# Kernel optimization log

Hardware: AMD Instinct MI355X
Metric: run time of the kernel (lower is better)

The kernel has to match this reference:

```python
import jax, jax.numpy as jnp
import numpy as np

B, T = 1, 2048
N_HEAD = 16
N_KV_HEAD = 16
N_EMBD = 1024
HEAD_DIM = N_EMBD // N_HEAD  # 64
HD8 = HEAD_DIM // 8          # 8 octonion blocks per head
EPS_RMS = 1e-6


def qconj(q):
    return q * jnp.array([1.0, -1.0, -1.0, -1.0], dtype=q.dtype)


def qmul(q1, q2):
    # Hamilton product, (...,4) x (...,4) -> (...,4)
    w1, x1, y1, z1 = (q1[..., 0], q1[..., 1], q1[..., 2], q1[..., 3])
    w2, x2, y2, z2 = (q2[..., 0], q2[..., 1], q2[..., 2], q2[..., 3])
    return jnp.stack([
        w1 * w2 - x1 * x2 - y1 * y2 - z1 * z2,
        w1 * x2 + x1 * w2 + y1 * z2 - z1 * y2,
        w1 * y2 - x1 * z2 + y1 * w2 + z1 * x2,
        w1 * z2 + x1 * y2 - y1 * x2 + z1 * w2,
    ], axis=-1)


def omul(o1, o2):
    # Cayley-Dickson octonion product, (...,8)
    a, b = o1[..., :4], o1[..., 4:]
    c, d = o2[..., :4], o2[..., 4:]
    first = qmul(a, c) - qmul(qconj(d), b)
    second = qmul(d, a) + qmul(b, qconj(c))
    return jnp.concatenate([first, second], axis=-1)


def oconj(o):
    return jnp.concatenate([qconj(o[..., :4]), -o[..., 4:]], axis=-1)


# Octonion multiplication structure constants: omul(x, y)[k] = x[a] y[p] C[a,p,k]
_EYE8 = jnp.eye(8, dtype=jnp.float32)
C_OCT = jax.vmap(lambda ei: jax.vmap(lambda ej: omul(ei, ej))(_EYE8))(_EYE8)  # (8,8,8)
# Trilinear tensor for omul(omul(q, kc), v):  T3[a,p,q,k] = sum_e C[a,p,e] C[e,q,k]
T3 = jnp.einsum('ape,eqk->apqk', C_OCT, C_OCT)  # (8,8,8,8)


def apply_rotary_emb(x, cos, sin):
    # x: (B, T, H, hd); cos/sin: (1, T, 1, hd//2)
    d = x.shape[-1] // 2
    x1, x2 = x[..., :d], x[..., d:]
    y1 = x1 * cos + x2 * sin
    y2 = x2 * cos - x1 * sin
    return jnp.concatenate([y1, y2], axis=-1)


def rms_norm(x):
    return x * jax.lax.rsqrt(jnp.mean(x * x, axis=-1, keepdims=True) + EPS_RMS)


def setup_inputs() -> dict:
    key = jax.random.key(0)
    ks = jax.random.split(key, 7)
    x = jax.random.normal(ks[0], (B, T, N_EMBD), dtype=jnp.float32)
    cos = jax.random.uniform(ks[1], (1, T, 1, HEAD_DIM // 2), dtype=jnp.float32)
    sin = jax.random.uniform(ks[2], (1, T, 1, HEAD_DIM // 2), dtype=jnp.float32)
    s = 0.02
    Wq = jax.random.normal(ks[3], (N_HEAD * HEAD_DIM, N_EMBD), dtype=jnp.float32) * s
    Wk = jax.random.normal(ks[4], (N_KV_HEAD * HEAD_DIM, N_EMBD), dtype=jnp.float32) * s
    Wv = jax.random.normal(ks[5], (N_KV_HEAD * HEAD_DIM, N_EMBD), dtype=jnp.float32) * s
    Wo = jax.random.normal(ks[6], (N_EMBD, N_EMBD), dtype=jnp.float32) * s
    return {"x": x, "cos": cos, "sin": sin, "Wq": Wq, "Wk": Wk, "Wv": Wv, "Wo": Wo}


def reference(x, cos, sin, Wq, Wk, Wv, Wo):
    Bx, Tx, Cx = x.shape
    q = (x @ Wq.T).reshape(Bx, Tx, N_HEAD, HEAD_DIM)
    k = (x @ Wk.T).reshape(Bx, Tx, N_KV_HEAD, HEAD_DIM)
    v = (x @ Wv.T).reshape(Bx, Tx, N_KV_HEAD, HEAD_DIM)
    q = rms_norm(apply_rotary_emb(q, cos, sin))
    k = rms_norm(apply_rotary_emb(k, cos, sin))
    q = q.transpose(0, 2, 1, 3)  # (B,H,T,hd)
    k = k.transpose(0, 2, 1, 3)
    v = v.transpose(0, 2, 1, 3)

    q_o = q.reshape(Bx, N_HEAD, Tx, HD8, 8)
    k_o = k.reshape(Bx, N_KV_HEAD, Tx, HD8, 8)
    v_o = v.reshape(Bx, N_KV_HEAD, Tx, HD8, 8)
    # F.normalize(p=2, dim=-1): divide by max(||.||, 1e-12)
    k_o = k_o / jnp.maximum(jnp.linalg.norm(k_o, axis=-1, keepdims=True), 1e-12)

    # Scores use the (pre-octonion-normalized) rotary+rms k
    scores = jnp.einsum('bhid,bhjd->bhij', q, k) * (HEAD_DIM ** -0.5)
    mask = jnp.tril(jnp.ones((Tx, Tx), dtype=bool))
    scores = jnp.where(mask, scores, -jnp.inf)
    probs = jax.nn.softmax(scores, axis=-1)  # (B,H,Tq,Tk)

    # y_i = sum_j p_ij * omul(omul(q_i, oconj(k_j)), v_j)
    # omul is bilinear, so pull the j-sum inside:
    # y_i[k] = q_i[a] * T3[a,p,c,k] * (sum_j p_ij kc_j[p] v_j[c])
    kc = oconj(k_o)                                              # (B,H,Tk,M,8)
    KV = jnp.einsum('bhjmp,bhjmq->bhjmpq', kc, v_o)              # (B,H,Tk,M,8,8)
    Z = jnp.einsum('bhij,bhjmpq->bhimpq', probs, KV)             # (B,H,Tq,M,8,8)
    y_o = jnp.einsum('bhima,apqk,bhimpq->bhimk', q_o, T3, Z)     # (B,H,Tq,M,8)

    y = y_o.reshape(Bx, N_HEAD, Tx, HEAD_DIM).transpose(0, 2, 1, 3).reshape(Bx, Tx, Cx)
    return y @ Wo.T
```

## Files before the change

kernel.cpp:

```cpp
#include <hip/hip_runtime.h>

typedef unsigned short u16;
typedef unsigned int u32;

#define T_SEQ 2048
#define NHEAD 16
#define HDIM 64
#define CDIM 1024
#define W_HSTR (512*2048)
#define Z_HSTR (2048*512)

#define SGBITS 0xB2D8741EACC66A00ULL

#define EXP2C 0.18033688011112042f

typedef _Float16 f16x8 __attribute__((ext_vector_type(8)));
typedef float f32x4 __attribute__((ext_vector_type(4)));

__device__ __forceinline__ float h2f(u16 u) { _Float16 h; __builtin_memcpy(&h, &u, 2); return (float)h; }
__device__ __forceinline__ u16 f2h(float f) { _Float16 h = (_Float16)f; u16 u; __builtin_memcpy(&u, &h, 2); return u; }
__device__ __forceinline__ u32 pk(float a, float b) { return (u32)f2h(a) | ((u32)f2h(b) << 16); }

__device__ __forceinline__ void gload16(const u16* g, u16* l) {
    __builtin_amdgcn_global_load_lds((const __attribute__((address_space(1))) u32*)g,
                                     (__attribute__((address_space(3))) u32*)l, 16, 0, 0);
}

template<bool F16OUT>
__device__ __forceinline__ void hgemm_tile(const u16* __restrict__ At, int lda,
                                           const u16* __restrict__ Bt, int ldb, int K,
                                           float* __restrict__ Cf, u16* __restrict__ Ch,
                                           int ldc, float scale, u16* As, u16* Bs) {
    int t = threadIdx.x;
    int wave = t >> 6, l = t & 63;
    int wm = wave & 1, wn = wave >> 1;
    int quad = l >> 4, lr = l & 15;
    f32x4 acc[4][4];
#pragma unroll
    for (int i = 0; i < 4; ++i)
#pragma unroll
        for (int j = 0; j < 4; ++j) acc[i][j] = (f32x4){0.f, 0.f, 0.f, 0.f};
    int acol = quad * 8;
    for (int k0 = 0; k0 < K; k0 += 64) {
#pragma unroll
        for (int j = 0; j < 4; ++j) {
            int d = wave * 4 + j;
            int kb = d >> 3, seg = d & 7;
            size_t roff = (size_t)(seg * 16 + lr);
            int coff = k0 + kb * 32 + acol;
            gload16(At + roff * lda + coff, As + d * 512);
            gload16(Bt + roff * ldb + coff, Bs + d * 512);
        }
        __syncthreads();
#pragma unroll
        for (int kb = 0; kb < 2; ++kb) {
            f16x8 af[4], bf[4];
#pragma unroll
            for (int mi = 0; mi < 4; ++mi) af[mi] = *(const f16x8*)&As[(kb * 8 + wm * 4 + mi) * 512 + l * 8];
#pragma unroll
            for (int ni = 0; ni < 4; ++ni) bf[ni] = *(const f16x8*)&Bs[(kb * 8 + wn * 4 + ni) * 512 + l * 8];
#pragma unroll
            for (int mi = 0; mi < 4; ++mi)
#pragma unroll
                for (int ni = 0; ni < 4; ++ni)
                    acc[mi][ni] = __builtin_amdgcn_mfma_f32_16x16x32_f16(af[mi], bf[ni], acc[mi][ni], 0, 0, 0);
        }
        __syncthreads();
    }
#pragma unroll
    for (int mi = 0; mi < 4; ++mi)
#pragma unroll
        for (int ni = 0; ni < 4; ++ni)
#pragma unroll
            for (int rr = 0; rr < 4; ++rr) {
                int gr = wm * 64 + mi * 16 + quad * 4 + rr;
                int gc = wn * 64 + ni * 16 + lr;
                float v = acc[mi][ni][rr] * scale;
                if (F16OUT) Ch[(size_t)gr * ldc + gc] = f2h(v);
                else Cf[(size_t)gr * ldc + gc] = v;
            }
}

__global__ __launch_bounds__(256) void hgemm_f32(const u16* __restrict__ A, int lda,
                                                 const u16* __restrict__ B, int ldb,
                                                 float* __restrict__ C, int ldc, int K) {
    __shared__ u16 As[8192], Bs[8192];
    int bm = blockIdx.y * 128, bn = blockIdx.x * 128;
    hgemm_tile<false>(A + (size_t)bm * lda, lda, B + (size_t)bn * ldb, ldb, K,
                      C + (size_t)bm * ldc + bn, nullptr, ldc, 1.f, As, Bs);
}

__global__ __launch_bounds__(256) void hgemm_f16(const u16* __restrict__ A, int lda,
                                                 const u16* __restrict__ B, int ldb,
                                                 u16* __restrict__ C, int ldc, int K) {
    __shared__ u16 As[8192], Bs[8192];
    int bm = blockIdx.y * 128, bn = blockIdx.x * 128;
    hgemm_tile<true>(A + (size_t)bm * lda, lda, B + (size_t)bn * ldb, ldb, K,
                     nullptr, C + (size_t)bm * ldc + bn, ldc, 1.f, As, Bs);
}

__global__ __launch_bounds__(256, 2) void flash_pw(const u16* __restrict__ q16,
                                                   const u16* __restrict__ k16,
                                                   const u16* __restrict__ W,
                                                   u16* __restrict__ Z,
                                                   float* __restrict__ lbuf) {
    __shared__ u16 Pl[2][128 * 136];
    int idx = blockIdx.x;
    int rb = 15 - (idx >> 6);
    int i6 = idx & 63;
    int h = ((i6 & 7) << 1) | ((i6 >> 3) & 1);
    int nq = i6 >> 4;
    int t = threadIdx.x;
    int wave = t >> 6, l = t & 63;
    int wm = wave & 1, wn = wave >> 1;
    int quad = l >> 4, lr = l & 15;

    const u16* qbase = q16 + (size_t)(rb * 128 + wm * 64 + lr) * CDIM + h * HDIM + quad * 8;
    f16x8 qa[4][2];
#pragma unroll
    for (int mi = 0; mi < 4; ++mi)
#pragma unroll
        for (int kb = 0; kb < 2; ++kb)
            qa[mi][kb] = *(const f16x8*)(qbase + (size_t)(mi * 16) * CDIM + kb * 32);

    f32x4 accz[4][4];
    f32x4 accl[4];
#pragma unroll
    for (int mi = 0; mi < 4; ++mi) {
        accl[mi] = (f32x4){0.f, 0.f, 0.f, 0.f};
#pragma unroll
        for (int ni = 0; ni < 4; ++ni) accz[mi][ni] = (f32x4){0.f, 0.f, 0.f, 0.f};
    }
    f16x8 ones;
#pragma unroll
    for (int j = 0; j < 8; ++j) ones[j] = (_Float16)1.0f;

    const u16* kbase = k16 + (size_t)(wn * 64 + lr) * CDIM + h * HDIM + quad * 8;
    const u16* Wbase = W + (size_t)h * W_HSTR + (size_t)(nq * 128 + wn * 64 + lr) * T_SEQ + quad * 8;

    auto qk = [&](int cb, f32x4 (&s)[4][4]) {
        f16x8 kf[4][2];
#pragma unroll
        for (int ni = 0; ni < 4; ++ni)
#pragma unroll
            for (int kb = 0; kb < 2; ++kb)
                kf[ni][kb] = *(const f16x8*)(kbase + (size_t)(cb * 128 + ni * 16) * CDIM + kb * 32);
#pragma unroll
        for (int mi = 0; mi < 4; ++mi)
#pragma unroll
            for (int ni = 0; ni < 4; ++ni) s[mi][ni] = (f32x4){0.f, 0.f, 0.f, 0.f};
#pragma unroll
        for (int kb = 0; kb < 2; ++kb)
#pragma unroll
            for (int mi = 0; mi < 4; ++mi)
#pragma unroll
                for (int ni = 0; ni < 4; ++ni)
                    s[mi][ni] = __builtin_amdgcn_mfma_f32_16x16x32_f16(qa[mi][kb], kf[ni][kb], s[mi][ni], 0, 0, 0);
    };
    auto expst = [&](int cb, f32x4 (&s)[4][4], u16* Pd) {
#pragma unroll
        for (int mi = 0; mi < 4; ++mi) {
            int row = wm * 64 + mi * 16 + quad * 4;
#pragma unroll
            for (int ni = 0; ni < 4; ++ni) {
                int col = wn * 64 + ni * 16 + lr;
#pragma unroll
                for (int rr = 0; rr < 4; ++rr) {
                    bool valid = (cb < rb) | (col <= row + rr);
                    float p = valid ? __builtin_amdgcn_exp2f(s[mi][ni][rr] * EXP2C - 12.f) : 0.f;
                    Pd[(row + rr) * 136 + col] = f2h(p);
                }
            }
        }
    };
    auto pw = [&](int cb, const u16* Ps) {
#pragma unroll
        for (int kb = 0; kb < 4; ++kb) {
            f16x8 pf[4], wf[4];
#pragma unroll
            for (int ni = 0; ni < 4; ++ni)
                wf[ni] = *(const f16x8*)(Wbase + (size_t)(ni * 16) * T_SEQ + cb * 128 + kb * 32);
#pragma unroll
            for (int mi = 0; mi < 4; ++mi)
                pf[mi] = *(const f16x8*)&Ps[(wm * 64 + mi * 16 + lr) * 136 + kb * 32 + quad * 8];
#pragma unroll
            for (int mi = 0; mi < 4; ++mi) {
#pragma unroll
                for (int ni = 0; ni < 4; ++ni)
                    accz[mi][ni] = __builtin_amdgcn_mfma_f32_16x16x32_f16(pf[mi], wf[ni], accz[mi][ni], 0, 0, 0);
                if (nq == 0)
                    accl[mi] = __builtin_amdgcn_mfma_f32_16x16x32_f16(pf[mi], ones, accl[mi], 0, 0, 0);
            }
        }
    };

    {
        f32x4 s[4][4];
        qk(0, s);
        expst(0, s, Pl[0]);
    }
    int cur = 0;
    for (int cb = 1; cb <= rb; ++cb) {
        __syncthreads();
        f32x4 s[4][4];
        qk(cb, s);
        pw(cb - 1, Pl[cur]);
        expst(cb, s, Pl[cur ^ 1]);
        cur ^= 1;
    }
    __syncthreads();
    pw(rb, Pl[cur]);

    u16* Zb = Z + (size_t)h * Z_HSTR;
#pragma unroll
    for (int mi = 0; mi < 4; ++mi)
#pragma unroll
        for (int rr = 0; rr < 4; ++rr) {
            int row = rb * 128 + wm * 64 + mi * 16 + quad * 4 + rr;
#pragma unroll
            for (int ni = 0; ni < 4; ++ni) {
                int col = nq * 128 + wn * 64 + ni * 16 + lr;
                Zb[(size_t)row * 512 + col] = f2h(accz[mi][ni][rr]);
            }
        }
    if (nq == 0 && lr == 0) {
#pragma unroll
        for (int mi = 0; mi < 4; ++mi) {
            int row = rb * 128 + wm * 64 + mi * 16 + quad * 4;
            *(f32x4*)(lbuf + h * T_SEQ + row) = accl[mi];
        }
    }
}

__global__ __launch_bounds__(256) void cvt5(const float* __restrict__ x, const float* __restrict__ wq,
                                            const float* __restrict__ wk, const float* __restrict__ wv,
                                            const float* __restrict__ wo,
                                            u16* __restrict__ x16, u16* __restrict__ w16) {
    int z = blockIdx.y;
    size_t base = ((size_t)blockIdx.x * 256 + threadIdx.x) * 8;
    const float* src;
    u16* dst;
    size_t cnt;
    if (z == 0) { src = x; dst = x16; cnt = 2097152; }
    else if (z == 1) { src = wq; dst = w16; cnt = 1048576; }
    else if (z == 2) { src = wk; dst = w16 + 1048576; cnt = 1048576; }
    else if (z == 3) { src = wv; dst = w16 + 2097152; cnt = 1048576; }
    else { src = wo; dst = w16 + 3145728; cnt = 1048576; }
    if (base >= cnt) return;
    float4 f0 = *(const float4*)(src + base);
    float4 f1 = *(const float4*)(src + base + 4);
    uint4 o;
    o.x = pk(f0.x, f0.y); o.y = pk(f0.z, f0.w); o.z = pk(f1.x, f1.y); o.w = pk(f1.z, f1.w);
    *(uint4*)(dst + base) = o;
}

__global__ __launch_bounds__(256) void prep_rope(const u16* __restrict__ qkv,
                                                 u16* __restrict__ q16, u16* __restrict__ k16,
                                                 float* __restrict__ kc,
                                                 const float* __restrict__ cosb, const float* __restrict__ sinb) {
    int wave = threadIdx.x >> 6, lane = threadIdx.x & 63;
    int idx = blockIdx.x * 4 + wave;
    int t = idx >> 4, h = idx & 15;
    int d = lane & 31;
    float cs = cosb[t * 32 + d];
    float sn = sinb[t * 32 + d];
    size_t b3 = (size_t)t * 3072 + h * HDIM;
    size_t b1 = (size_t)t * CDIM + h * HDIM;

    float xq = h2f(qkv[b3 + lane]);
    float oq = __shfl(xq, lane ^ 32);
    float rq = (lane < 32) ? fmaf(xq, cs, oq * sn) : fmaf(xq, cs, -oq * sn);
    float ssq = rq * rq;
#pragma unroll
    for (int m = 1; m < 64; m <<= 1) ssq += __shfl_xor(ssq, m);
    rq *= rsqrtf(ssq * (1.f / 64.f) + 1e-6f);
    q16[b1 + lane] = f2h(rq);

    float xk = h2f(qkv[b3 + 1024 + lane]);
    float ok = __shfl(xk, lane ^ 32);
    float rk = (lane < 32) ? fmaf(xk, cs, ok * sn) : fmaf(xk, cs, -ok * sn);
    float ssk = rk * rk;
#pragma unroll
    for (int m = 1; m < 64; m <<= 1) ssk += __shfl_xor(ssk, m);
    rk *= rsqrtf(ssk * (1.f / 64.f) + 1e-6f);
    k16[b1 + lane] = f2h(rk);

    float s8 = rk * rk;
    s8 += __shfl_xor(s8, 1); s8 += __shfl_xor(s8, 2); s8 += __shfl_xor(s8, 4);
    float sc2 = 1.f / fmaxf(sqrtf(s8), 1e-12f);
    float kcv = rk * sc2;
    if (lane & 7) kcv = -kcv;
    kc[b1 + lane] = kcv;
}

__global__ __launch_bounds__(256) void w_pre(const float* __restrict__ kc, const u16* __restrict__ qkv,
                                             u16* __restrict__ W) {
    __shared__ float kcs[64][65];
    __shared__ float vs[64][65];
    int h = blockIdx.y;
    int j0 = blockIdx.x * 64;
    int t = threadIdx.x;
    int r = t >> 2, cq = (t & 3) * 16;
    const float* kp = kc + (size_t)(j0 + r) * CDIM + h * HDIM + cq;
    const u16* vp = qkv + (size_t)(j0 + r) * 3072 + 2048 + h * HDIM + cq;
#pragma unroll
    for (int u4 = 0; u4 < 4; ++u4) {
        float4 a = *(const float4*)(kp + u4 * 4);
        ushort4 b = *(const ushort4*)(vp + u4 * 4);
        kcs[r][cq + u4 * 4 + 0] = a.x; kcs[r][cq + u4 * 4 + 1] = a.y;
        kcs[r][cq + u4 * 4 + 2] = a.z; kcs[r][cq + u4 * 4 + 3] = a.w;
        vs[r][cq + u4 * 4 + 0] = h2f(b.x); vs[r][cq + u4 * 4 + 1] = h2f(b.y);
        vs[r][cq + u4 * 4 + 2] = h2f(b.z); vs[r][cq + u4 * 4 + 3] = h2f(b.w);
    }
    __syncthreads();
    int j = t & 63, g = t >> 6;
    u16* Wp = W + (size_t)h * W_HSTR + j0 + j;
    for (int ae = g * 16; ae < g * 16 + 16; ++ae) {
        int a = ae >> 3, e = ae & 7;
        u32 mask = 0;
#pragma unroll
        for (int qq = 0; qq < 8; ++qq) {
            int p = a ^ e ^ qq;
            u32 bit = (u32)(((SGBITS >> (a * 8 + p)) ^ (SGBITS >> ((e ^ qq) * 8 + qq))) & 1ULL);
            mask |= bit << qq;
        }
#pragma unroll
        for (int m = 0; m < 8; ++m) {
            float w = 0.f;
#pragma unroll
            for (int qq = 0; qq < 8; ++qq) {
                float t1 = kcs[j][m * 8 + (a ^ e ^ qq)] * vs[j][m * 8 + qq];
                w = ((mask >> qq) & 1) ? (w - t1) : (w + t1);
            }
            Wp[(size_t)(m * 64 + ae) * T_SEQ] = f2h(w);
        }
    }
}

__global__ __launch_bounds__(256) void contract_y(const u16* __restrict__ q16, const u16* __restrict__ Z,
                                                  const float* __restrict__ lbuf, u16* __restrict__ y16) {
    __shared__ u16 zb[4][512];
    int wave = threadIdx.x >> 6, lane = threadIdx.x & 63;
    int idx = blockIdx.x * 4 + wave;
    int i = idx >> 4, h = idx & 15;
    uint4 zv = *(const uint4*)(Z + (size_t)h * Z_HSTR + (size_t)i * 512 + lane * 8);
    *(uint4*)&zb[wave][lane * 8] = zv;
    int m = lane >> 3, e = lane & 7;
    const u16* qp = q16 + (size_t)i * CDIM + h * HDIM + m * 8;
    uint4 qb = *(const uint4*)qp;
    float qv[8];
    qv[0] = h2f(qb.x & 0xffff); qv[1] = h2f(qb.x >> 16);
    qv[2] = h2f(qb.y & 0xffff); qv[3] = h2f(qb.y >> 16);
    qv[4] = h2f(qb.z & 0xffff); qv[5] = h2f(qb.z >> 16);
    qv[6] = h2f(qb.w & 0xffff); qv[7] = h2f(qb.w >> 16);
    float linv = 1.f / lbuf[h * T_SEQ + i];
    __syncthreads();
    float acc = 0.f;
#pragma unroll
    for (int a = 0; a < 8; ++a) acc = fmaf(qv[a], h2f(zb[wave][m * 64 + a * 8 + e]), acc);
    y16[(size_t)i * CDIM + h * HDIM + lane] = f2h(acc * linv);
}

extern "C" void kernel_launch(void* const* d_in, const int* in_sizes, int n_in,
                              void* d_out, int out_size, void* d_ws, size_t ws_size,
                              hipStream_t stream) {
    const float* x = (const float*)d_in[0];
    const float* cosb = (const float*)d_in[1];
    const float* sinb = (const float*)d_in[2];
    const float* Wq = (const float*)d_in[3];
    const float* Wk = (const float*)d_in[4];
    const float* Wv = (const float*)d_in[5];
    const float* Wo = (const float*)d_in[6];
    float* out = (float*)d_out;
    char* base = (char*)d_ws;
    u16* qkv16 = (u16*)base;
    float* kc = (float*)(base + 12582912);
    u16* x16 = (u16*)(base + 20971520);
    u16* w16 = (u16*)(base + 25165824);
    u16* q16 = (u16*)(base + 33554432);
    u16* k16 = (u16*)(base + 37748736);
    u16* y16 = (u16*)(base + 41943040);
    u16* W = (u16*)(base + 46137344);
    u16* Z = (u16*)(base + 79691776);
    float* lbuf = (float*)(base + 113246208);

    cvt5<<<dim3(1024, 5), 256, 0, stream>>>(x, Wq, Wk, Wv, Wo, x16, w16);
    hgemm_f16<<<dim3(24, 16), 256, 0, stream>>>(x16, CDIM, w16, CDIM, qkv16, 3072, CDIM);
    prep_rope<<<T_SEQ * NHEAD / 4, 256, 0, stream>>>(qkv16, q16, k16, kc, cosb, sinb);
    w_pre<<<dim3(32, 16), 256, 0, stream>>>(kc, qkv16, W);
    flash_pw<<<1024, 256, 0, stream>>>(q16, k16, W, Z, lbuf);
    contract_y<<<NHEAD * T_SEQ / 4, 256, 0, stream>>>(q16, Z, lbuf, y16);
    hgemm_f32<<<dim3(8, 16), 256, 0, stream>>>(y16, CDIM, w16 + 3145728, CDIM, out, CDIM, CDIM);
}
```

Before: 304.0 us.

## Halve flash_pw query tile to 64 rows with transposed, XOR-swizzled P staging

Each flash_pw block now covers 64 query rows instead of 128, which doubles the grid to 2048 blocks and halves the per-block register accumulators. QK^T is computed transposed (K as the A operand), so each lane writes 4 contiguous P values as one ushort4 into an XOR-swizzled LDS layout, replacing the padded scalar stores. The aim is more parallelism, less register pressure, better causal load balance and fewer LDS bank conflicts. In exchange, the QK^T work and K/W global loads are duplicated across twice as many blocks.

After: 381.1 us. 1.25x slower.

```diff
diff --git a/kernel.cpp b/kernel.cpp
--- a/kernel.cpp
+++ b/kernel.cpp
@@ -104,29 +104,32 @@
                                                    const u16* __restrict__ W,
                                                    u16* __restrict__ Z,
                                                    float* __restrict__ lbuf) {
-    __shared__ u16 Pl[2][128 * 136];
+    __shared__ u16 Pt[2][64 * 128];
     int idx = blockIdx.x;
-    int rb = 15 - (idx >> 6);
-    int i6 = idx & 63;
-    int h = ((i6 & 7) << 1) | ((i6 >> 3) & 1);
-    int nq = i6 >> 4;
+    int rb = 15 - (idx >> 7);
+    int sub = idx & 127;
+    int h = ((sub & 7) << 1) | ((sub >> 3) & 1);
+    int nq = (sub >> 4) & 3;
+    int ih = sub >> 6;
     int t = threadIdx.x;
     int wave = t >> 6, l = t & 63;
-    int wm = wave & 1, wn = wave >> 1;
     int quad = l >> 4, lr = l & 15;
-
-    const u16* qbase = q16 + (size_t)(rb * 128 + wm * 64 + lr) * CDIM + h * HDIM + quad * 8;
-    f16x8 qa[4][2];
-#pragma unroll
-    for (int mi = 0; mi < 4; ++mi)
+    int wj = wave & 1, wiq = wave >> 1;
+    int wi = wave & 1, wn = wave >> 1;
+    int i0 = rb * 128 + ih * 64;
+
+    const u16* qb = q16 + (size_t)(i0 + wiq * 32 + lr) * CDIM + h * HDIM + quad * 8;
+    f16x8 qa[2][2];
+#pragma unroll
+    for (int ni = 0; ni < 2; ++ni)
 #pragma unroll
         for (int kb = 0; kb < 2; ++kb)
-            qa[mi][kb] = *(const f16x8*)(qbase + (size_t)(mi * 16) * CDIM + kb * 32);
-
-    f32x4 accz[4][4];
-    f32x4 accl[4];
-#pragma unroll
-    for (int mi = 0; mi < 4; ++mi) {
+            qa[ni][kb] = *(const f16x8*)(qb + (size_t)(ni * 16) * CDIM + kb * 32);
+
+    f32x4 accz[2][4];
+    f32x4 accl[2];
+#pragma unroll
+    for (int mi = 0; mi < 2; ++mi) {
         accl[mi] = (f32x4){0.f, 0.f, 0.f, 0.f};
 #pragma unroll
         for (int ni = 0; ni < 4; ++ni) accz[mi][ni] = (f32x4){0.f, 0.f, 0.f, 0.f};
@@ -135,98 +138,105 @@
 #pragma unroll
     for (int j = 0; j < 8; ++j) ones[j] = (_Float16)1.0f;
 
-    const u16* kbase = k16 + (size_t)(wn * 64 + lr) * CDIM + h * HDIM + quad * 8;
+    const u16* kbase = k16 + (size_t)(wj * 64 + lr) * CDIM + h * HDIM + quad * 8;
     const u16* Wbase = W + (size_t)h * W_HSTR + (size_t)(nq * 128 + wn * 64 + lr) * T_SEQ + quad * 8;
 
-    auto qk = [&](int cb, f32x4 (&s)[4][4]) {
+    auto qk = [&](int cb, f32x4 (&s)[4][2]) {
         f16x8 kf[4][2];
 #pragma unroll
-        for (int ni = 0; ni < 4; ++ni)
+        for (int mi = 0; mi < 4; ++mi)
 #pragma unroll
             for (int kb = 0; kb < 2; ++kb)
-                kf[ni][kb] = *(const f16x8*)(kbase + (size_t)(cb * 128 + ni * 16) * CDIM + kb * 32);
+                kf[mi][kb] = *(const f16x8*)(kbase + (size_t)(cb * 128 + mi * 16) * CDIM + kb * 32);
 #pragma unroll
         for (int mi = 0; mi < 4; ++mi)
 #pragma unroll
-            for (int ni = 0; ni < 4; ++ni) s[mi][ni] = (f32x4){0.f, 0.f, 0.f, 0.f};
+            for (int ni = 0; ni < 2; ++ni) s[mi][ni] = (f32x4){0.f, 0.f, 0.f, 0.f};
 #pragma unroll
         for (int kb = 0; kb < 2; ++kb)
 #pragma unroll
             for (int mi = 0; mi < 4; ++mi)
 #pragma unroll
-                for (int ni = 0; ni < 4; ++ni)
-                    s[mi][ni] = __builtin_amdgcn_mfma_f32_16x16x32_f16(qa[mi][kb], kf[ni][kb], s[mi][ni], 0, 0, 0);
+                for (int ni = 0; ni < 2; ++ni)
+                    s[mi][ni] = __builtin_amdgcn_mfma_f32_16x16x32_f16(kf[mi][kb], qa[ni][kb], s[mi][ni], 0, 0, 0);
     };
-    auto expst = [&](int cb, f32x4 (&s)[4][4], u16* Pd) {
+    auto expst = [&](int cb, f32x4 (&s)[4][2], u16* Pd) {
 #pragma unroll
         for (int mi = 0; mi < 4; ++mi) {
-            int row = wm * 64 + mi * 16 + quad * 4;
-#pragma unroll
-            for (int ni = 0; ni < 4; ++ni) {
-                int col = wn * 64 + ni * 16 + lr;
+            int j0 = wj * 64 + mi * 16 + quad * 4;
+            int chunk = j0 >> 3, joff = j0 & 7;
+#pragma unroll
+            for (int ni = 0; ni < 2; ++ni) {
+                int iloc = wiq * 32 + ni * 16 + lr;
+                ushort4 o;
+                u16* pr = (u16*)&o;
 #pragma unroll
                 for (int rr = 0; rr < 4; ++rr) {
-                    bool valid = (cb < rb) | (col <= row + rr);
+                    bool valid = (cb < rb) | ((j0 + rr) <= (ih * 64 + iloc));
                     float p = valid ? __builtin_amdgcn_exp2f(s[mi][ni][rr] * EXP2C - 12.f) : 0.f;
-                    Pd[(row + rr) * 136 + col] = f2h(p);
+                    pr[rr] = f2h(p);
                 }
+                *(ushort4*)&Pd[iloc * 128 + ((chunk ^ (iloc & 15)) << 3) + joff] = o;
             }
         }
     };
     auto pw = [&](int cb, const u16* Ps) {
 #pragma unroll
         for (int kb = 0; kb < 4; ++kb) {
-            f16x8 pf[4], wf[4];
+            f16x8 pf[2], wf[4];
 #pragma unroll
             for (int ni = 0; ni < 4; ++ni)
                 wf[ni] = *(const f16x8*)(Wbase + (size_t)(ni * 16) * T_SEQ + cb * 128 + kb * 32);
 #pragma unroll
-            for (int mi = 0; mi < 4; ++mi)
-                pf[mi] = *(const f16x8*)&Ps[(wm * 64 + mi * 16 + lr) * 136 + kb * 32 + quad * 8];
-#pragma unroll
-            for (int mi = 0; mi < 4; ++mi) {
+            for (int mi = 0; mi < 2; ++mi) {
+                int iloc = wi * 32 + mi * 16 + lr;
+                int chunk = kb * 4 + quad;
+                pf[mi] = *(const f16x8*)&Ps[iloc * 128 + ((chunk ^ (iloc & 15)) << 3)];
+            }
+#pragma unroll
+            for (int mi = 0; mi < 2; ++mi) {
 #pragma unroll
                 for (int ni = 0; ni < 4; ++ni)
                     accz[mi][ni] = __builtin_amdgcn_mfma_f32_16x16x32_f16(pf[mi], wf[ni], accz[mi][ni], 0, 0, 0);
-                if (nq == 0)
+                if (nq == 0 && wn == 0)
                     accl[mi] = __builtin_amdgcn_mfma_f32_16x16x32_f16(pf[mi], ones, accl[mi], 0, 0, 0);
             }
         }
     };
 
     {
-        f32x4 s[4][4];
+        f32x4 s[4][2];
         qk(0, s);
-        expst(0, s, Pl[0]);
+        expst(0, s, Pt[0]);
     }
     int cur = 0;
     for (int cb = 1; cb <= rb; ++cb) {
         __syncthreads();
-        f32x4 s[4][4];
+        f32x4 s[4][2];
         qk(cb, s);
-        pw(cb - 1, Pl[cur]);
-        expst(cb, s, Pl[cur ^ 1]);
+        pw(cb - 1, Pt[cur]);
+        expst(cb, s, Pt[cur ^ 1]);
         cur ^= 1;
     }
     __syncthreads();
-    pw(rb, Pl[cur]);
+    pw(rb, Pt[cur]);
 
     u16* Zb = Z + (size_t)h * Z_HSTR;
 #pragma unroll
-    for (int mi = 0; mi < 4; ++mi)
+    for (int mi = 0; mi < 2; ++mi)
 #pragma unroll
         for (int rr = 0; rr < 4; ++rr) {
-            int row = rb * 128 + wm * 64 + mi * 16 + quad * 4 + rr;
+            int row = i0 + wi * 32 + mi * 16 + quad * 4 + rr;
 #pragma unroll
             for (int ni = 0; ni < 4; ++ni) {
                 int col = nq * 128 + wn * 64 + ni * 16 + lr;
                 Zb[(size_t)row * 512 + col] = f2h(accz[mi][ni][rr]);
             }
         }
-    if (nq == 0 && lr == 0) {
-#pragma unroll
-        for (int mi = 0; mi < 4; ++mi) {
-            int row = rb * 128 + wm * 64 + mi * 16 + quad * 4;
+    if (nq == 0 && wn == 0 && lr == 0) {
+#pragma unroll
+        for (int mi = 0; mi < 2; ++mi) {
+            int row = i0 + wi * 32 + mi * 16 + quad * 4;
             *(f32x4*)(lbuf + h * T_SEQ + row) = accl[mi];
         }
     }
@@ -388,7 +398,7 @@
     hgemm_f16<<<dim3(24, 16), 256, 0, stream>>>(x16, CDIM, w16, CDIM, qkv16, 3072, CDIM);
     prep_rope<<<T_SEQ * NHEAD / 4, 256, 0, stream>>>(qkv16, q16, k16, kc, cosb, sinb);
     w_pre<<<dim3(32, 16), 256, 0, stream>>>(kc, qkv16, W);
-    flash_pw<<<1024, 256, 0, stream>>>(q16, k16, W, Z, lbuf);
+    flash_pw<<<2048, 256, 0, stream>>>(q16, k16, W, Z, lbuf);
     contract_y<<<NHEAD * T_SEQ / 4, 256, 0, stream>>>(q16, Z, lbuf, y16);
     hgemm_f32<<<dim3(8, 16), 256, 0, stream>>>(y16, CDIM, w16 + 3145728, CDIM, out, CDIM, CDIM);
 }
```

## Fuse octonion q-contraction epilogue into flash_pw and drop contract_y kernel

Applied to the files above, without the earlier changes.

The final contraction of q with the accumulated Z tile and the division by the row sum now happen inside the flash kernel's epilogue. The Z tile is staged through shared memory, transposed with a padded stride, and each block computes its two octonion blocks of y directly. This removes the global Z buffer write and read (about 32 MB of fp16 traffic), the lbuf round trip, and a separate kernel launch. In exchange, every block now computes the row-sum MFMA instead of only nq==0 blocks, and the epilogue adds extra syncs and LDS traffic that may see bank conflicts.

New measurement: 339.5 us. 11.7% more time.

```diff
diff --git a/kernel.cpp b/kernel.cpp
--- a/kernel.cpp
+++ b/kernel.cpp
@@ -8,7 +8,6 @@
 #define HDIM 64
 #define CDIM 1024
 #define W_HSTR (512*2048)
-#define Z_HSTR (2048*512)
 
 #define SGBITS 0xB2D8741EACC66A00ULL
 
@@ -102,8 +101,7 @@
 __global__ __launch_bounds__(256, 2) void flash_pw(const u16* __restrict__ q16,
                                                    const u16* __restrict__ k16,
                                                    const u16* __restrict__ W,
-                                                   u16* __restrict__ Z,
-                                                   float* __restrict__ lbuf) {
+                                                   u16* __restrict__ y16) {
     __shared__ u16 Pl[2][128 * 136];
     int idx = blockIdx.x;
     int rb = 15 - (idx >> 6);
@@ -188,8 +186,7 @@
 #pragma unroll
                 for (int ni = 0; ni < 4; ++ni)
                     accz[mi][ni] = __builtin_amdgcn_mfma_f32_16x16x32_f16(pf[mi], wf[ni], accz[mi][ni], 0, 0, 0);
-                if (nq == 0)
-                    accl[mi] = __builtin_amdgcn_mfma_f32_16x16x32_f16(pf[mi], ones, accl[mi], 0, 0, 0);
+                accl[mi] = __builtin_amdgcn_mfma_f32_16x16x32_f16(pf[mi], ones, accl[mi], 0, 0, 0);
             }
         }
     };
@@ -211,25 +208,39 @@
     __syncthreads();
     pw(rb, Pl[cur]);
 
-    u16* Zb = Z + (size_t)h * Z_HSTR;
+    __syncthreads();
+    u16* Zl = (u16*)Pl;
 #pragma unroll
     for (int mi = 0; mi < 4; ++mi)
 #pragma unroll
         for (int rr = 0; rr < 4; ++rr) {
-            int row = rb * 128 + wm * 64 + mi * 16 + quad * 4 + rr;
+            int row = wm * 64 + mi * 16 + quad * 4 + rr;
+            float inv = 1.f / accl[mi][rr];
 #pragma unroll
             for (int ni = 0; ni < 4; ++ni) {
-                int col = nq * 128 + wn * 64 + ni * 16 + lr;
-                Zb[(size_t)row * 512 + col] = f2h(accz[mi][ni][rr]);
-            }
-        }
-    if (nq == 0 && lr == 0) {
-#pragma unroll
-        for (int mi = 0; mi < 4; ++mi) {
-            int row = rb * 128 + wm * 64 + mi * 16 + quad * 4;
-            *(f32x4*)(lbuf + h * T_SEQ + row) = accl[mi];
-        }
-    }
+                int col = wn * 64 + ni * 16 + lr;
+                Zl[col * 137 + row] = f2h(accz[mi][ni][rr] * inv);
+            }
+        }
+    __syncthreads();
+    int mloc = t >> 7, i = t & 127;
+    const u16* qp2 = q16 + (size_t)(rb * 128 + i) * CDIM + h * HDIM + (nq * 2 + mloc) * 8;
+    uint4 qb2 = *(const uint4*)qp2;
+    float qv[8];
+    qv[0] = h2f(qb2.x & 0xffff); qv[1] = h2f(qb2.x >> 16);
+    qv[2] = h2f(qb2.y & 0xffff); qv[3] = h2f(qb2.y >> 16);
+    qv[4] = h2f(qb2.z & 0xffff); qv[5] = h2f(qb2.z >> 16);
+    qv[6] = h2f(qb2.w & 0xffff); qv[7] = h2f(qb2.w >> 16);
+    u16 outs[8];
+#pragma unroll
+    for (int e = 0; e < 8; ++e) {
+        float acc = 0.f;
+#pragma unroll
+        for (int a = 0; a < 8; ++a)
+            acc = fmaf(qv[a], h2f(Zl[(mloc * 64 + a * 8 + e) * 137 + i]), acc);
+        outs[e] = f2h(acc);
+    }
+    *(uint4*)(y16 + (size_t)(rb * 128 + i) * CDIM + h * HDIM + (nq * 2 + mloc) * 8) = *(uint4*)outs;
 }
 
 __global__ __launch_bounds__(256) void cvt5(const float* __restrict__ x, const float* __restrict__ wq,
@@ -337,30 +348,6 @@
     }
 }
 
-__global__ __launch_bounds__(256) void contract_y(const u16* __restrict__ q16, const u16* __restrict__ Z,
-                                                  const float* __restrict__ lbuf, u16* __restrict__ y16) {
-    __shared__ u16 zb[4][512];
-    int wave = threadIdx.x >> 6, lane = threadIdx.x & 63;
-    int idx = blockIdx.x * 4 + wave;
-    int i = idx >> 4, h = idx & 15;
-    uint4 zv = *(const uint4*)(Z + (size_t)h * Z_HSTR + (size_t)i * 512 + lane * 8);
-    *(uint4*)&zb[wave][lane * 8] = zv;
-    int m = lane >> 3, e = lane & 7;
-    const u16* qp = q16 + (size_t)i * CDIM + h * HDIM + m * 8;
-    uint4 qb = *(const uint4*)qp;
-    float qv[8];
-    qv[0] = h2f(qb.x & 0xffff); qv[1] = h2f(qb.x >> 16);
-    qv[2] = h2f(qb.y & 0xffff); qv[3] = h2f(qb.y >> 16);
-    qv[4] = h2f(qb.z & 0xffff); qv[5] = h2f(qb.z >> 16);
-    qv[6] = h2f(qb.w & 0xffff); qv[7] = h2f(qb.w >> 16);
-    float linv = 1.f / lbuf[h * T_SEQ + i];
-    __syncthreads();
-    float acc = 0.f;
-#pragma unroll
-    for (int a = 0; a < 8; ++a) acc = fmaf(qv[a], h2f(zb[wave][m * 64 + a * 8 + e]), acc);
-    y16[(size_t)i * CDIM + h * HDIM + lane] = f2h(acc * linv);
-}
-
 extern "C" void kernel_launch(void* const* d_in, const int* in_sizes, int n_in,
                               void* d_out, int out_size, void* d_ws, size_t ws_size,
                               hipStream_t stream) {
@@ -381,14 +368,11 @@
     u16* k16 = (u16*)(base + 37748736);
     u16* y16 = (u16*)(base + 41943040);
     u16* W = (u16*)(base + 46137344);
-    u16* Z = (u16*)(base + 79691776);
-    float* lbuf = (float*)(base + 113246208);
 
     cvt5<<<dim3(1024, 5), 256, 0, stream>>>(x, Wq, Wk, Wv, Wo, x16, w16);
     hgemm_f16<<<dim3(24, 16), 256, 0, stream>>>(x16, CDIM, w16, CDIM, qkv16, 3072, CDIM);
     prep_rope<<<T_SEQ * NHEAD / 4, 256, 0, stream>>>(qkv16, q16, k16, kc, cosb, sinb);
     w_pre<<<dim3(32, 16), 256, 0, stream>>>(kc, qkv16, W);
-    flash_pw<<<1024, 256, 0, stream>>>(q16, k16, W, Z, lbuf);
-    contract_y<<<NHEAD * T_SEQ / 4, 256, 0, stream>>>(q16, Z, lbuf, y16);
+    flash_pw<<<1024, 256, 0, stream>>>(q16, k16, W, y16);
     hgemm_f32<<<dim3(8, 16), 256, 0, stream>>>(y16, CDIM, w16 + 3145728, CDIM, out, CDIM, CDIM);
 }
```
